# Optimization experiments

Hardware: AMD Instinct MI355X
Metric: run time of the kernel (lower is better)

The kernel has to match this reference:

```python
import jax, jax.numpy as jnp
import numpy as np

B, Q, S, D = 16, 2048, 2048, 128  # batch(*heads), q_len, kv seq_len, dim_q_k == dim_v


def setup_inputs() -> dict:
    key = jax.random.key(0)
    k1, k2, k3, k4 = jax.random.split(key, 4)
    value = jax.random.normal(k1, (B, S, D), dtype=jnp.float32)
    k_ = jax.random.normal(k2, (B, S, D), dtype=jnp.float32)
    query = jax.random.normal(k3, (B, Q, D), dtype=jnp.float32)
    mask = jax.random.bernoulli(k4, 0.5, (B, Q, S))  # True = illegal connection
    return {"value": value, "key": k_, "query": query, "mask": mask}


def reference(value, key, query, mask):
    scale = np.power(D, -0.5).astype(np.float32)
    # adjacency: [B, Q, S]
    adjacency = jnp.einsum('bqd,bsd->bqs', query, key) * scale
    adjacency = jnp.where(mask, -jnp.inf, adjacency)
    attention = jax.nn.softmax(adjacency, axis=2)
    out = jnp.einsum('bqs,bsd->bqd', attention, value)
    return (out, attention)
```

## Files before the change

### kernel.cpp

```cpp
#include <hip/hip_runtime.h>
#include <hip/hip_bf16.h>

#define B_ 16
#define Q_ 2048
#define S_ 2048
#define D_ 128
#define SCALE 0.08838834764831845f

typedef unsigned short ushort_t;
typedef unsigned long long u64_t;
typedef __attribute__((ext_vector_type(8))) __bf16 bf16x8;
typedef __attribute__((ext_vector_type(8))) short short8;
typedef __attribute__((ext_vector_type(4))) float floatx4;

static __device__ __forceinline__ ushort_t bf16_of_f32(float f) {
    __hip_bfloat16 h = __float2bfloat16(f);
    return *reinterpret_cast<ushort_t*>(&h);
}
static __device__ __forceinline__ float f32_of_bf16(ushort_t u) {
    return __uint_as_float(((unsigned int)u) << 16);
}

__global__ void detect_kernel(const unsigned int* __restrict__ m,
                              const unsigned int* __restrict__ q,
                              int* __restrict__ flags) {
    __shared__ int sI32, sF32, sF16, sCnt;
    int t = threadIdx.x;
    if (t == 0) { sI32 = 0; sF32 = 0; sF16 = 0; sCnt = 0; }
    __syncthreads();
    int notI32 = 0, notF32 = 0, notF16 = 0;
    for (int i = t; i < 1024; i += 256) {
        unsigned int v = m[i];
        if (v & ~1u) notI32 = 1;
        if (!(v == 0u || v == 0x3F800000u)) notF32 = 1;
        unsigned int h0 = v & 0xFFFFu, h1 = v >> 16;
        if (!(h0 == 0u || h0 == 0x3F80u || h0 == 0x3C00u)) notF16 = 1;
        if (!(h1 == 0u || h1 == 0x3F80u || h1 == 0x3C00u)) notF16 = 1;
    }
    int cnt = 0;
    for (int i = t; i < 4096; i += 256) {
        unsigned int lo = q[i] & 0xFFFFu;
        unsigned int e = (lo >> 7) & 0xFFu;
        if (lo == 0u || (e >= 100u && e <= 140u)) cnt++;
    }
    if (notI32) atomicOr(&sI32, 1);
    if (notF32) atomicOr(&sF32, 1);
    if (notF16) atomicOr(&sF16, 1);
    atomicAdd(&sCnt, cnt);
    __syncthreads();
    if (t == 0) {
        int w;
        if (!sI32)      w = 4;
        else if (!sF32) w = 4;
        else if (!sF16) w = 2;
        else            w = 1;
        flags[0] = w;
        flags[1] = (sCnt >= 3276) ? 0 : 1;
    }
}

__global__ void convert_bf16_kernel(const float* __restrict__ src,
                                    const int* __restrict__ flags,
                                    ushort_t* __restrict__ dst) {
    if (flags[1] == 0) return;
    size_t i = ((size_t)blockIdx.x * 256 + threadIdx.x) * 8;
    float4 f0 = *(const float4*)(src + i);
    float4 f1 = *(const float4*)(src + i + 4);
    short8 w;
    w[0] = (short)bf16_of_f32(f0.x); w[1] = (short)bf16_of_f32(f0.y);
    w[2] = (short)bf16_of_f32(f0.z); w[3] = (short)bf16_of_f32(f0.w);
    w[4] = (short)bf16_of_f32(f1.x); w[5] = (short)bf16_of_f32(f1.y);
    w[6] = (short)bf16_of_f32(f1.z); w[7] = (short)bf16_of_f32(f1.w);
    *(short8*)(dst + i) = w;
}

__global__ void transpose_v_kernel(const void* __restrict__ Vraw,
                                   const int* __restrict__ flags,
                                   ushort_t* __restrict__ Vt) {
    __shared__ ushort_t t[32][33];
    const int dt = flags[1];
    int b = blockIdx.z;
    int sb = blockIdx.x * 32, db = blockIdx.y * 32;
    int x = threadIdx.x, y = threadIdx.y;
    ushort_t* Vtb = Vt + (size_t)b * D_ * S_;
    if (dt == 0) {
        const ushort_t* Vb = (const ushort_t*)Vraw + (size_t)b * S_ * D_;
        #pragma unroll
        for (int i = 0; i < 32; i += 8)
            t[y + i][x] = Vb[(size_t)(sb + y + i) * D_ + db + x];
    } else {
        const float* Vb = (const float*)Vraw + (size_t)b * S_ * D_;
        #pragma unroll
        for (int i = 0; i < 32; i += 8)
            t[y + i][x] = bf16_of_f32(Vb[(size_t)(sb + y + i) * D_ + db + x]);
    }
    __syncthreads();
    #pragma unroll
    for (int i = 0; i < 32; i += 8)
        Vtb[(size_t)(db + y + i) * S_ + sb + x] = t[x][y + i];
}

__launch_bounds__(512, 4)
__global__ void attn_fused_kernel(const void* __restrict__ Kraw,
                                  const ushort_t* __restrict__ Kbf,
                                  const void* __restrict__ Qraw,
                                  const void* __restrict__ maskp,
                                  const int* __restrict__ flags,
                                  const ushort_t* __restrict__ Vt,
                                  u64_t* __restrict__ bits,
                                  void* __restrict__ out_base) {
    __shared__ __align__(16) char smem[62976];
    ushort_t (*Kl)[136] = (ushort_t(*)[136])smem;
    ushort_t (*Vl)[72]  = (ushort_t(*)[72])(smem + 17408);
    float    (*Ob)[132] = (float(*)[132])smem;
    ushort_t (*El)[72]  = (ushort_t(*)[72])(smem + 35840);
    char*    Mlb        = smem + 45056;
    float*   lpart      = (float*)(smem + 62464);

    const int tid  = threadIdx.x;
    const int wave = tid >> 6;
    const int lane = tid & 63;
    const int quad = lane >> 4;
    const int c    = lane & 15;
    const int sh   = wave & 1;
    const int wg   = wave >> 1;

    const int qt = blockIdx.x, b = blockIdx.y;
    const int q0 = qt * 64;
    const int mw = flags[0];
    const int dt = flags[1];

    const ushort_t* Kp = dt ? Kbf : (const ushort_t*)Kraw;

    ushort_t* outh  = (ushort_t*)out_base;
    float*    outf  = (float*)out_base;
    ushort_t* attnh = outh + (size_t)B_ * Q_ * D_;
    float*    attnf = outf + (size_t)B_ * Q_ * D_;

    const size_t rowbase = (size_t)b * Q_ + q0;
    const int myrow = wg * 16 + quad * 4;

    bf16x8 qf[4];
    {
        const size_t qrow = rowbase + wg * 16 + c;
        if (dt == 0) {
            const ushort_t* p = (const ushort_t*)Qraw + qrow * D_;
            #pragma unroll
            for (int kk = 0; kk < 4; ++kk)
                qf[kk] = *(const bf16x8*)(p + kk * 32 + quad * 8);
        } else {
            const float* p = (const float*)Qraw + qrow * D_;
            #pragma unroll
            for (int kk = 0; kk < 4; ++kk) {
                float4 f0 = *(const float4*)(p + kk * 32 + quad * 8);
                float4 f1 = *(const float4*)(p + kk * 32 + quad * 8 + 4);
                bf16x8 w;
                w[0] = (__bf16)f0.x; w[1] = (__bf16)f0.y;
                w[2] = (__bf16)f0.z; w[3] = (__bf16)f0.w;
                w[4] = (__bf16)f1.x; w[5] = (__bf16)f1.y;
                w[6] = (__bf16)f1.z; w[7] = (__bf16)f1.w;
                qf[kk] = w;
            }
        }
    }

    floatx4 accO[8];
    #pragma unroll
    for (int i = 0; i < 8; ++i) accO[i] = (floatx4){0.f, 0.f, 0.f, 0.f};
    float lacc[4] = {0.f, 0.f, 0.f, 0.f};

    for (int s0 = 0; s0 < S_; s0 += 64) {
        __syncthreads();
        #pragma unroll
        for (int j = 0; j < 2; ++j) {
            int i = tid + 512 * j;
            int row = i >> 4, cg = i & 15;
            *(short8*)(&Kl[row][cg * 8]) =
                *(const short8*)(Kp + (size_t)(b * S_ + s0 + row) * D_ + cg * 8);
        }
        #pragma unroll
        for (int j = 0; j < 2; ++j) {
            int i = tid + 512 * j;
            int row = i >> 3, cg = i & 7;
            *(short8*)(&Vl[row][cg * 8]) =
                *(const short8*)(Vt + (size_t)(b * D_ + row) * S_ + s0 + cg * 8);
        }
        if (mw == 4) {
            const unsigned int* Mg = (const unsigned int*)maskp;
            #pragma unroll
            for (int j = 0; j < 2; ++j) {
                int i = tid + 512 * j;
                int row = i >> 4, c4 = i & 15;
                *(uint4*)(Mlb + row * 272 + c4 * 16) =
                    *(const uint4*)(Mg + (rowbase + row) * (size_t)S_ + s0 + c4 * 4);
            }
        } else if (mw == 2) {
            const ushort_t* Mg = (const ushort_t*)maskp;
            int row = tid >> 3, c16 = tid & 7;
            *(uint4*)(Mlb + row * 272 + c16 * 16) =
                *(const uint4*)(Mg + (rowbase + row) * (size_t)S_ + s0 + c16 * 8);
        } else {
            if (tid < 256) {
                const unsigned char* Mg = (const unsigned char*)maskp;
                int row = tid >> 2, c16 = tid & 3;
                *(uint4*)(Mlb + row * 272 + c16 * 16) =
                    *(const uint4*)(Mg + (rowbase + row) * (size_t)S_ + s0 + c16 * 16);
            }
        }
        __syncthreads();

        #pragma unroll
        for (int k = 0; k < 8; ++k) {
            int row = wave * 8 + k;
            bool mk;
            if (mw == 4)      mk = ((const unsigned int*)(Mlb + row * 272))[lane] != 0u;
            else if (mw == 2) mk = ((const ushort_t*)(Mlb + row * 272))[lane] != 0;
            else              mk = ((const unsigned char*)(Mlb + row * 272))[lane] != 0;
            u64_t bm = __ballot(mk);
            if (lane == 0) bits[(rowbase + row) * 32 + (s0 >> 6)] = bm;
        }

        #pragma unroll
        for (int sti = 0; sti < 2; ++sti) {
            const int st = sh * 2 + sti;
            floatx4 acc = (floatx4){0.f, 0.f, 0.f, 0.f};
            #pragma unroll
            for (int kk = 0; kk < 4; ++kk) {
                bf16x8 bf = *(const bf16x8*)(&Kl[st * 16 + c][kk * 32 + quad * 8]);
                acc = __builtin_amdgcn_mfma_f32_16x16x32_bf16(qf[kk], bf, acc, 0, 0, 0);
            }
            #pragma unroll
            for (int r = 0; r < 4; ++r) {
                const int row = myrow + r, col = st * 16 + c;
                bool masked;
                if (mw == 4)      masked = ((const unsigned int*)(Mlb + row * 272))[col] != 0u;
                else if (mw == 2) masked = ((const ushort_t*)(Mlb + row * 272))[col] != 0;
                else              masked = ((const unsigned char*)(Mlb + row * 272))[col] != 0;
                float e = masked ? 0.f : __expf(acc[r] * SCALE);
                lacc[r] += e;
                El[row][col] = bf16_of_f32(e);
            }
        }
        {
            bf16x8 af = *(const bf16x8*)(&El[wg * 16 + c][sh * 32 + quad * 8]);
            #pragma unroll
            for (int nt = 0; nt < 8; ++nt) {
                bf16x8 bv = *(const bf16x8*)(&Vl[nt * 16 + c][sh * 32 + quad * 8]);
                accO[nt] = __builtin_amdgcn_mfma_f32_16x16x32_bf16(af, bv, accO[nt], 0, 0, 0);
            }
        }
    }

    #pragma unroll
    for (int r = 0; r < 4; ++r) {
        float v = lacc[r];
        v += __shfl_xor(v, 1); v += __shfl_xor(v, 2);
        v += __shfl_xor(v, 4); v += __shfl_xor(v, 8);
        lacc[r] = v;
    }
    __syncthreads();
    if (c == 0) {
        #pragma unroll
        for (int r = 0; r < 4; ++r) lpart[sh * 64 + myrow + r] = lacc[r];
    }
    __syncthreads();
    float rcpl[4];
    #pragma unroll
    for (int r = 0; r < 4; ++r)
        rcpl[r] = 1.0f / fmaxf(lpart[myrow + r] + lpart[64 + myrow + r], 1e-30f);

    if (sh == 0) {
        #pragma unroll
        for (int r = 0; r < 4; ++r)
            #pragma unroll
            for (int nt = 0; nt < 8; ++nt)
                Ob[myrow + r][nt * 16 + c] = accO[nt][r];
    }
    __syncthreads();
    if (sh == 1) {
        #pragma unroll
        for (int r = 0; r < 4; ++r)
            #pragma unroll
            for (int nt = 0; nt < 8; ++nt)
                Ob[myrow + r][nt * 16 + c] += accO[nt][r];
    }
    __syncthreads();
    {
        const int row = tid >> 3, dc = tid & 7;
        float rcp = 1.0f / fmaxf(lpart[row] + lpart[64 + row], 1e-30f);
        size_t obase = (rowbase + row) * (size_t)D_ + dc * 16;
        if (dt == 0) {
            short8 w0, w1;
            #pragma unroll
            for (int k = 0; k < 8; ++k) {
                w0[k] = (short)bf16_of_f32(Ob[row][dc * 16 + k] * rcp);
                w1[k] = (short)bf16_of_f32(Ob[row][dc * 16 + 8 + k] * rcp);
            }
            *(short8*)(outh + obase) = w0;
            *(short8*)(outh + obase + 8) = w1;
        } else {
            #pragma unroll
            for (int g = 0; g < 4; ++g) {
                float4 f;
                f.x = Ob[row][dc * 16 + g * 4 + 0] * rcp;
                f.y = Ob[row][dc * 16 + g * 4 + 1] * rcp;
                f.z = Ob[row][dc * 16 + g * 4 + 2] * rcp;
                f.w = Ob[row][dc * 16 + g * 4 + 3] * rcp;
                *(float4*)(outf + obase + g * 4) = f;
            }
        }
    }

    for (int s0 = 0; s0 < S_; s0 += 64) {
        __syncthreads();
        #pragma unroll
        for (int j = 0; j < 2; ++j) {
            int i = tid + 512 * j;
            int row = i >> 4, cg = i & 15;
            *(short8*)(&Kl[row][cg * 8]) =
                *(const short8*)(Kp + (size_t)(b * S_ + s0 + row) * D_ + cg * 8);
        }
        __syncthreads();

        u64_t bw[4];
        #pragma unroll
        for (int r = 0; r < 4; ++r)
            bw[r] = bits[(rowbase + myrow + r) * 32 + (s0 >> 6)];

        #pragma unroll
        for (int sti = 0; sti < 2; ++sti) {
            const int st = sh * 2 + sti;
            floatx4 acc = (floatx4){0.f, 0.f, 0.f, 0.f};
            #pragma unroll
            for (int kk = 0; kk < 4; ++kk) {
                bf16x8 bf = *(const bf16x8*)(&Kl[st * 16 + c][kk * 32 + quad * 8]);
                acc = __builtin_amdgcn_mfma_f32_16x16x32_bf16(qf[kk], bf, acc, 0, 0, 0);
            }
            #pragma unroll
            for (int r = 0; r < 4; ++r) {
                bool masked = (bw[r] >> (st * 16 + c)) & 1ull;
                float e = masked ? 0.f : __expf(acc[r] * SCALE) * rcpl[r];
                El[myrow + r][st * 16 + c] = bf16_of_f32(e);
            }
        }
        __syncthreads();

        {
            const int row = tid >> 3, sc = tid & 7;
            short8 v = *(short8*)(&El[row][sc * 8]);
            size_t gidx = (rowbase + row) * (size_t)S_ + s0 + sc * 8;
            if (dt == 0) {
                *(short8*)(attnh + gidx) = v;
            } else {
                float4 f0, f1;
                f0.x = f32_of_bf16((ushort_t)v[0]); f0.y = f32_of_bf16((ushort_t)v[1]);
                f0.z = f32_of_bf16((ushort_t)v[2]); f0.w = f32_of_bf16((ushort_t)v[3]);
                f1.x = f32_of_bf16((ushort_t)v[4]); f1.y = f32_of_bf16((ushort_t)v[5]);
                f1.z = f32_of_bf16((ushort_t)v[6]); f1.w = f32_of_bf16((ushort_t)v[7]);
                *(float4*)(attnf + gidx) = f0;
                *(float4*)(attnf + gidx + 4) = f1;
            }
        }
    }
}

extern "C" void kernel_launch(void* const* d_in, const int* in_sizes, int n_in,
                              void* d_out, int out_size, void* d_ws, size_t ws_size,
                              hipStream_t stream) {
    const void* Vraw = d_in[0];
    const void* Kraw = d_in[1];
    const void* Qraw = d_in[2];
    const void* maskp = d_in[3];

    char* ws = (char*)d_ws;
    int*  flags   = (int*)ws;
    ushort_t* Vt  = (ushort_t*)(ws + 256);
    u64_t* bits   = (u64_t*)(ws + 256 + 8388608);
    ushort_t* Kbf = (ushort_t*)(ws + 256 + 2 * 8388608);

    detect_kernel<<<1, 256, 0, stream>>>((const unsigned int*)maskp,
                                         (const unsigned int*)Qraw, flags);
    convert_bf16_kernel<<<(B_ * S_ * D_) / 2048, 256, 0, stream>>>(
        (const float*)Kraw, flags, Kbf);
    transpose_v_kernel<<<dim3(S_ / 32, D_ / 32, B_), dim3(32, 8), 0, stream>>>(
        Vraw, flags, Vt);
    attn_fused_kernel<<<dim3(Q_ / 64, B_), 512, 0, stream>>>(
        Kraw, Kbf, Qraw, maskp, flags, Vt, bits, d_out);
}
```

Before: 607.6 us.

## Pack mask in separate kernel and double-buffer K/V via direct global-to-LDS loads

Mask bit-packing moves out of the fused attention kernel into a dedicated kernel, so the main loops read only 64-bit mask words. K and V tiles are now loaded with global_load_lds straight into a double-buffered, XOR-swizzled LDS layout, so the next tile's loads overlap the current tile's MFMA work. The second pass also double-buffers the normalized probability tile, letting each tile's global store overlap the next tile's compute. In exchange, LDS use grows, which may lower occupancy, and an extra kernel launch plus a full pass over the mask is added.

```diff
diff --git a/kernel.cpp b/kernel.cpp
--- a/kernel.cpp
+++ b/kernel.cpp
@@ -19,6 +19,11 @@
 }
 static __device__ __forceinline__ float f32_of_bf16(ushort_t u) {
     return __uint_as_float(((unsigned int)u) << 16);
+}
+static __device__ __forceinline__ void gload_lds16(const void* g, void* l) {
+    __builtin_amdgcn_global_load_lds(
+        (const __attribute__((address_space(1))) unsigned int*)g,
+        (__attribute__((address_space(3))) unsigned int*)l, 16, 0, 0);
 }
 
 __global__ void detect_kernel(const unsigned int* __restrict__ m,
@@ -100,22 +105,62 @@
         Vtb[(size_t)(db + y + i) * S_ + sb + x] = t[x][y + i];
 }
 
+__global__ void mask_pack_kernel(const void* __restrict__ maskp,
+                                 const int* __restrict__ flags,
+                                 u64_t* __restrict__ bits) {
+    const int mw = flags[0];
+    const int lane = threadIdx.x & 63;
+    const size_t row = (size_t)blockIdx.x * 4 + (threadIdx.x >> 6);
+    for (int seg = 0; seg < 4; ++seg) {
+        const size_t col = (size_t)seg * 512 + lane * 8;
+        unsigned int b8 = 0;
+        if (mw == 1) {
+            u64_t v = *(const u64_t*)((const unsigned char*)maskp + row * S_ + col);
+            #pragma unroll
+            for (int j = 0; j < 8; ++j)
+                b8 |= (unsigned int)(((v >> (8 * j)) & 0xFFull) != 0ull) << j;
+        } else if (mw == 2) {
+            const ushort_t* p = (const ushort_t*)maskp + row * S_ + col;
+            uint4 v = *(const uint4*)p;
+            const unsigned int* w = (const unsigned int*)&v;
+            #pragma unroll
+            for (int j = 0; j < 4; ++j) {
+                b8 |= (unsigned int)((w[j] & 0xFFFFu) != 0u) << (2 * j);
+                b8 |= (unsigned int)((w[j] >> 16) != 0u) << (2 * j + 1);
+            }
+        } else {
+            const unsigned int* p = (const unsigned int*)maskp + row * S_ + col;
+            uint4 v0 = *(const uint4*)p;
+            uint4 v1 = *(const uint4*)(p + 4);
+            const unsigned int* w0 = (const unsigned int*)&v0;
+            const unsigned int* w1 = (const unsigned int*)&v1;
+            #pragma unroll
+            for (int j = 0; j < 4; ++j) {
+                b8 |= (unsigned int)(w0[j] != 0u) << j;
+                b8 |= (unsigned int)(w1[j] != 0u) << (4 + j);
+            }
+        }
+        u64_t w = (u64_t)b8 << ((lane & 7) * 8);
+        w |= __shfl_xor(w, 1);
+        w |= __shfl_xor(w, 2);
+        w |= __shfl_xor(w, 4);
+        if ((lane & 7) == 0)
+            bits[row * 32 + seg * 8 + (lane >> 3)] = w;
+    }
+}
+
 __launch_bounds__(512, 4)
 __global__ void attn_fused_kernel(const void* __restrict__ Kraw,
                                   const ushort_t* __restrict__ Kbf,
                                   const void* __restrict__ Qraw,
-                                  const void* __restrict__ maskp,
                                   const int* __restrict__ flags,
                                   const ushort_t* __restrict__ Vt,
-                                  u64_t* __restrict__ bits,
+                                  const u64_t* __restrict__ bits,
                                   void* __restrict__ out_base) {
-    __shared__ __align__(16) char smem[62976];
-    ushort_t (*Kl)[136] = (ushort_t(*)[136])smem;
-    ushort_t (*Vl)[72]  = (ushort_t(*)[72])(smem + 17408);
-    float    (*Ob)[132] = (float(*)[132])smem;
-    ushort_t (*El)[72]  = (ushort_t(*)[72])(smem + 35840);
-    char*    Mlb        = smem + 45056;
-    float*   lpart      = (float*)(smem + 62464);
+    __shared__ __align__(16) char smem[75264];
+    ushort_t* El     = (ushort_t*)(smem + 65536);
+    float*    lpart  = (float*)(smem + 74752);
+    float (*Ob)[132] = (float(*)[132])smem;
 
     const int tid  = threadIdx.x;
     const int wave = tid >> 6;
@@ -127,7 +172,6 @@
 
     const int qt = blockIdx.x, b = blockIdx.y;
     const int q0 = qt * 64;
-    const int mw = flags[0];
     const int dt = flags[1];
 
     const ushort_t* Kp = dt ? Kbf : (const ushort_t*)Kraw;
@@ -139,6 +183,24 @@
 
     const size_t rowbase = (size_t)b * Q_ + q0;
     const int myrow = wg * 16 + quad * 4;
+    const u64_t* bb = bits + (rowbase + myrow) * 32;
+
+    const int kg0 = wave * 8 + (lane >> 4);
+    const int kg1 = wave * 8 + 4 + (lane >> 4);
+    const char* kp0 = (const char*)(Kp + (size_t)b * S_ * D_) + kg0 * 256
+                      + (((lane & 15) ^ (kg0 & 15)) << 4);
+    const char* kp1 = (const char*)(Kp + (size_t)b * S_ * D_) + kg1 * 256
+                      + (((lane & 15) ^ (kg1 & 15)) << 4);
+    const int vg0 = wave * 16 + (lane >> 3);
+    const int vg1 = wave * 16 + 8 + (lane >> 3);
+    const char* vp0 = (const char*)(Vt + ((size_t)b * D_ + vg0) * S_)
+                      + (((lane & 7) ^ (vg0 & 7)) << 4);
+    const char* vp1 = (const char*)(Vt + ((size_t)b * D_ + vg1) * S_)
+                      + (((lane & 7) ^ (vg1 & 7)) << 4);
+    char* kd0 = smem + wave * 2048;
+    char* kd1 = smem + wave * 2048 + 1024;
+    char* vd0 = smem + 32768 + wave * 2048;
+    char* vd1 = smem + 32768 + wave * 2048 + 1024;
 
     bf16x8 qf[4];
     {
@@ -169,86 +231,67 @@
     for (int i = 0; i < 8; ++i) accO[i] = (floatx4){0.f, 0.f, 0.f, 0.f};
     float lacc[4] = {0.f, 0.f, 0.f, 0.f};
 
-    for (int s0 = 0; s0 < S_; s0 += 64) {
-        __syncthreads();
-        #pragma unroll
-        for (int j = 0; j < 2; ++j) {
-            int i = tid + 512 * j;
-            int row = i >> 4, cg = i & 15;
-            *(short8*)(&Kl[row][cg * 8]) =
-                *(const short8*)(Kp + (size_t)(b * S_ + s0 + row) * D_ + cg * 8);
-        }
-        #pragma unroll
-        for (int j = 0; j < 2; ++j) {
-            int i = tid + 512 * j;
-            int row = i >> 3, cg = i & 7;
-            *(short8*)(&Vl[row][cg * 8]) =
-                *(const short8*)(Vt + (size_t)(b * D_ + row) * S_ + s0 + cg * 8);
-        }
-        if (mw == 4) {
-            const unsigned int* Mg = (const unsigned int*)maskp;
-            #pragma unroll
-            for (int j = 0; j < 2; ++j) {
-                int i = tid + 512 * j;
-                int row = i >> 4, c4 = i & 15;
-                *(uint4*)(Mlb + row * 272 + c4 * 16) =
-                    *(const uint4*)(Mg + (rowbase + row) * (size_t)S_ + s0 + c4 * 4);
-            }
-        } else if (mw == 2) {
-            const ushort_t* Mg = (const ushort_t*)maskp;
-            int row = tid >> 3, c16 = tid & 7;
-            *(uint4*)(Mlb + row * 272 + c16 * 16) =
-                *(const uint4*)(Mg + (rowbase + row) * (size_t)S_ + s0 + c16 * 8);
-        } else {
-            if (tid < 256) {
-                const unsigned char* Mg = (const unsigned char*)maskp;
-                int row = tid >> 2, c16 = tid & 3;
-                *(uint4*)(Mlb + row * 272 + c16 * 16) =
-                    *(const uint4*)(Mg + (rowbase + row) * (size_t)S_ + s0 + c16 * 16);
-            }
-        }
-        __syncthreads();
-
-        #pragma unroll
-        for (int k = 0; k < 8; ++k) {
-            int row = wave * 8 + k;
-            bool mk;
-            if (mw == 4)      mk = ((const unsigned int*)(Mlb + row * 272))[lane] != 0u;
-            else if (mw == 2) mk = ((const ushort_t*)(Mlb + row * 272))[lane] != 0;
-            else              mk = ((const unsigned char*)(Mlb + row * 272))[lane] != 0;
-            u64_t bm = __ballot(mk);
-            if (lane == 0) bits[(rowbase + row) * 32 + (s0 >> 6)] = bm;
-        }
+    gload_lds16(kp0, kd0);
+    gload_lds16(kp1, kd1);
+    gload_lds16(vp0, vd0);
+    gload_lds16(vp1, vd1);
+    u64_t bw[4];
+    #pragma unroll
+    for (int r = 0; r < 4; ++r) bw[r] = bb[r * 32];
+    __syncthreads();
+
+    int cur = 0;
+    for (int t = 0; t < 32; ++t) {
+        const int nxt = cur ^ 1;
+        if (t + 1 < 32) {
+            const size_t ko = (size_t)(t + 1) << 14;
+            const size_t vo = (size_t)(t + 1) << 7;
+            gload_lds16(kp0 + ko, kd0 + nxt * 16384);
+            gload_lds16(kp1 + ko, kd1 + nxt * 16384);
+            gload_lds16(vp0 + vo, vd0 + nxt * 16384);
+            gload_lds16(vp1 + vo, vd1 + nxt * 16384);
+        }
+        const int tn = (t + 1 < 32) ? t + 1 : t;
+        u64_t bwn[4];
+        #pragma unroll
+        for (int r = 0; r < 4; ++r) bwn[r] = bb[r * 32 + tn];
+
+        const char* Klc = smem + cur * 16384;
+        const char* Vlc = smem + 32768 + cur * 16384;
 
         #pragma unroll
         for (int sti = 0; sti < 2; ++sti) {
             const int st = sh * 2 + sti;
+            const int krow = st * 16 + c;
+            const int rb = (krow & 15) << 4;
             floatx4 acc = (floatx4){0.f, 0.f, 0.f, 0.f};
             #pragma unroll
             for (int kk = 0; kk < 4; ++kk) {
-                bf16x8 bf = *(const bf16x8*)(&Kl[st * 16 + c][kk * 32 + quad * 8]);
+                bf16x8 bf = *(const bf16x8*)(Klc + krow * 256 + ((kk * 64 + quad * 16) ^ rb));
                 acc = __builtin_amdgcn_mfma_f32_16x16x32_bf16(qf[kk], bf, acc, 0, 0, 0);
             }
             #pragma unroll
             for (int r = 0; r < 4; ++r) {
-                const int row = myrow + r, col = st * 16 + c;
-                bool masked;
-                if (mw == 4)      masked = ((const unsigned int*)(Mlb + row * 272))[col] != 0u;
-                else if (mw == 2) masked = ((const ushort_t*)(Mlb + row * 272))[col] != 0;
-                else              masked = ((const unsigned char*)(Mlb + row * 272))[col] != 0;
+                bool masked = (bw[r] >> (st * 16 + c)) & 1ull;
                 float e = masked ? 0.f : __expf(acc[r] * SCALE);
                 lacc[r] += e;
-                El[row][col] = bf16_of_f32(e);
+                El[(myrow + r) * 72 + st * 16 + c] = bf16_of_f32(e);
             }
         }
         {
-            bf16x8 af = *(const bf16x8*)(&El[wg * 16 + c][sh * 32 + quad * 8]);
+            bf16x8 af = *(const bf16x8*)(El + (wg * 16 + c) * 72 + sh * 32 + quad * 8);
             #pragma unroll
             for (int nt = 0; nt < 8; ++nt) {
-                bf16x8 bv = *(const bf16x8*)(&Vl[nt * 16 + c][sh * 32 + quad * 8]);
+                const int vrow = nt * 16 + c;
+                const int vb = ((sh * 4 + quad) ^ (vrow & 7)) << 4;
+                bf16x8 bv = *(const bf16x8*)(Vlc + vrow * 128 + vb);
                 accO[nt] = __builtin_amdgcn_mfma_f32_16x16x32_bf16(af, bv, accO[nt], 0, 0, 0);
             }
         }
+        __syncthreads();
+        #pragma unroll
+        for (int r = 0; r < 4; ++r) bw[r] = bwn[r];
+        cur = nxt;
     }
 
     #pragma unroll
@@ -258,7 +301,6 @@
         v += __shfl_xor(v, 4); v += __shfl_xor(v, 8);
         lacc[r] = v;
     }
-    __syncthreads();
     if (c == 0) {
         #pragma unroll
         for (int r = 0; r < 4; ++r) lpart[sh * 64 + myrow + r] = lacc[r];
@@ -311,44 +353,32 @@
         }
     }
 
-    for (int s0 = 0; s0 < S_; s0 += 64) {
-        __syncthreads();
-        #pragma unroll
-        for (int j = 0; j < 2; ++j) {
-            int i = tid + 512 * j;
-            int row = i >> 4, cg = i & 15;
-            *(short8*)(&Kl[row][cg * 8]) =
-                *(const short8*)(Kp + (size_t)(b * S_ + s0 + row) * D_ + cg * 8);
-        }
-        __syncthreads();
-
-        u64_t bw[4];
-        #pragma unroll
-        for (int r = 0; r < 4; ++r)
-            bw[r] = bits[(rowbase + myrow + r) * 32 + (s0 >> 6)];
-
-        #pragma unroll
-        for (int sti = 0; sti < 2; ++sti) {
-            const int st = sh * 2 + sti;
-            floatx4 acc = (floatx4){0.f, 0.f, 0.f, 0.f};
-            #pragma unroll
-            for (int kk = 0; kk < 4; ++kk) {
-                bf16x8 bf = *(const bf16x8*)(&Kl[st * 16 + c][kk * 32 + quad * 8]);
-                acc = __builtin_amdgcn_mfma_f32_16x16x32_bf16(qf[kk], bf, acc, 0, 0, 0);
-            }
-            #pragma unroll
-            for (int r = 0; r < 4; ++r) {
-                bool masked = (bw[r] >> (st * 16 + c)) & 1ull;
-                float e = masked ? 0.f : __expf(acc[r] * SCALE) * rcpl[r];
-                El[myrow + r][st * 16 + c] = bf16_of_f32(e);
-            }
-        }
-        __syncthreads();
-
-        {
+    __syncthreads();
+    gload_lds16(kp0, kd0);
+    gload_lds16(kp1, kd1);
+    u64_t bw2[4];
+    #pragma unroll
+    for (int r = 0; r < 4; ++r) bw2[r] = bb[r * 32];
+    __syncthreads();
+
+    int cur2 = 0;
+    for (int t = 0; t < 32; ++t) {
+        const int nxt = cur2 ^ 1;
+        if (t + 1 < 32) {
+            const size_t ko = (size_t)(t + 1) << 14;
+            gload_lds16(kp0 + ko, kd0 + nxt * 16384);
+            gload_lds16(kp1 + ko, kd1 + nxt * 16384);
+        }
+        const int tn = (t + 1 < 32) ? t + 1 : t;
+        u64_t bwn[4];
+        #pragma unroll
+        for (int r = 0; r < 4; ++r) bwn[r] = bb[r * 32 + tn];
+
+        if (t > 0) {
+            const ushort_t* E2 = (const ushort_t*)(smem + 32768 + nxt * 16384);
             const int row = tid >> 3, sc = tid & 7;
-            short8 v = *(short8*)(&El[row][sc * 8]);
-            size_t gidx = (rowbase + row) * (size_t)S_ + s0 + sc * 8;
+            short8 v = *(const short8*)(E2 + row * 72 + sc * 8);
+            size_t gidx = (rowbase + row) * (size_t)S_ + (size_t)(t - 1) * 64 + sc * 8;
             if (dt == 0) {
                 *(short8*)(attnh + gidx) = v;
             } else {
@@ -361,6 +391,48 @@
                 *(float4*)(attnf + gidx + 4) = f1;
             }
         }
+
+        const char* Klc = smem + cur2 * 16384;
+        ushort_t* E2w = (ushort_t*)(smem + 32768 + cur2 * 16384);
+        #pragma unroll
+        for (int sti = 0; sti < 2; ++sti) {
+            const int st = sh * 2 + sti;
+            const int krow = st * 16 + c;
+            const int rb = (krow & 15) << 4;
+            floatx4 acc = (floatx4){0.f, 0.f, 0.f, 0.f};
+            #pragma unroll
+            for (int kk = 0; kk < 4; ++kk) {
+                bf16x8 bf = *(const bf16x8*)(Klc + krow * 256 + ((kk * 64 + quad * 16) ^ rb));
+                acc = __builtin_amdgcn_mfma_f32_16x16x32_bf16(qf[kk], bf, acc, 0, 0, 0);
+            }
+            #pragma unroll
+            for (int r = 0; r < 4; ++r) {
+                bool masked = (bw2[r] >> (st * 16 + c)) & 1ull;
+                float e = masked ? 0.f : __expf(acc[r] * SCALE) * rcpl[r];
+                E2w[(myrow + r) * 72 + st * 16 + c] = bf16_of_f32(e);
+            }
+        }
+        __syncthreads();
+        #pragma unroll
+        for (int r = 0; r < 4; ++r) bw2[r] = bwn[r];
+        cur2 = nxt;
+    }
+    {
+        const ushort_t* E2 = (const ushort_t*)(smem + 32768 + 16384);
+        const int row = tid >> 3, sc = tid & 7;
+        short8 v = *(const short8*)(E2 + row * 72 + sc * 8);
+        size_t gidx = (rowbase + row) * (size_t)S_ + (size_t)31 * 64 + sc * 8;
+        if (dt == 0) {
+            *(short8*)(attnh + gidx) = v;
+        } else {
+            float4 f0, f1;
+            f0.x = f32_of_bf16((ushort_t)v[0]); f0.y = f32_of_bf16((ushort_t)v[1]);
+            f0.z = f32_of_bf16((ushort_t)v[2]); f0.w = f32_of_bf16((ushort_t)v[3]);
+            f1.x = f32_of_bf16((ushort_t)v[4]); f1.y = f32_of_bf16((ushort_t)v[5]);
+            f1.z = f32_of_bf16((ushort_t)v[6]); f1.w = f32_of_bf16((ushort_t)v[7]);
+            *(float4*)(attnf + gidx) = f0;
+            *(float4*)(attnf + gidx + 4) = f1;
+        }
     }
 }
 
@@ -384,6 +456,7 @@
         (const float*)Kraw, flags, Kbf);
     transpose_v_kernel<<<dim3(S_ / 32, D_ / 32, B_), dim3(32, 8), 0, stream>>>(
         Vraw, flags, Vt);
+    mask_pack_kernel<<<(B_ * Q_) / 4, 256, 0, stream>>>(maskp, flags, bits);
     attn_fused_kernel<<<dim3(Q_ / 64, B_), 512, 0, stream>>>(
-        Kraw, Kbf, Qraw, maskp, flags, Vt, bits, d_out);
-}
+        Kraw, Kbf, Qraw, flags, Vt, bits, d_out);
+}
```

Result: no change. 598.1 us (-1.6%).
